# Kernel tuning notes

Hardware: AMD Instinct MI355X
Metric: run time of the kernel (lower is better)

Reference implementation:

```python
import jax, jax.numpy as jnp
import numpy as np

E = 1024   # embed_dim
H = 16     # num_heads
D = E // H # head_dim = 64
Q = 4      # num_queries
B = 4
S = 2048


def setup_inputs() -> dict:
    key = jax.random.key(0)
    ks = jax.random.split(key, 9)
    s = 0.02  # init scale for weights
    return {
        "x":  jax.random.normal(ks[0], (B, S, E), jnp.float32),
        "Wq": jax.random.normal(ks[1], (Q, E, E), jnp.float32) * s,  # stacked per-query Linear weights (torch layout: out,in)
        "bq": jax.random.normal(ks[2], (Q, E), jnp.float32) * s,
        "Wk": jax.random.normal(ks[3], (E, E), jnp.float32) * s,
        "bk": jax.random.normal(ks[4], (E,), jnp.float32) * s,
        "Wv": jax.random.normal(ks[5], (E, E), jnp.float32) * s,
        "bv": jax.random.normal(ks[6], (E,), jnp.float32) * s,
        "Wo": jax.random.normal(ks[7], (E, E), jnp.float32) * s,
        "bo": jax.random.normal(ks[8], (E,), jnp.float32) * s,
    }


def reference(x, Wq, bq, Wk, bk, Wv, bv, Wo, bo):
    B_, S_, E_ = x.shape
    scale = 1.0 / jnp.sqrt(jnp.asarray(D, x.dtype))
    # all query projections at once: (Q,B,S,E) -> (Q,B,S,H,D)
    q = (jnp.einsum('bse,qfe->qbsf', x, Wq) + bq[:, None, None, :]).reshape(Q, B_, S_, H, D)
    k = (x @ Wk.T + bk).reshape(B_, S_, H, D)
    v = (x @ Wv.T + bv).reshape(B_, S_, H, D)
    # NOTE: faithful to the torch code, which never moves the head axis before matmul:
    # scores[q,b,s,h,g] = sum_d q[q,b,s,h,d] * k[b,s,g,d]  -> softmax over heads g
    scores = jnp.einsum('qbshd,bsgd->qbshg', q, k) * scale      # (Q,B,S,H,H)
    probs = jax.nn.softmax(scores, axis=-1)
    out = jnp.einsum('qbshg,bsgd->qbshd', probs, v)             # (Q,B,S,H,D)
    # torch: .transpose(1,2).contiguous().view(B,S,E) == permute to (B,H,S,D) then reshape
    out = jnp.transpose(out, (0, 1, 3, 2, 4)).reshape(Q, B_, S_, E_)
    out = out.sum(axis=0)
    return out @ Wo.T + bo
```

## Files before the change

kernel.cpp:

```cpp
#include <hip/hip_runtime.h>


typedef __bf16 bf16x8 __attribute__((ext_vector_type(8)));
typedef float f32x4 __attribute__((ext_vector_type(4)));
typedef float f32x16 __attribute__((ext_vector_type(16)));

__device__ __forceinline__ unsigned short f2b(float f) {
  unsigned u = __float_as_uint(f);
  return (unsigned short)((u + 0x7fffu + ((u >> 16) & 1u)) >> 16);
}

__device__ __forceinline__ void async16(const void* g, void* l) {
  __builtin_amdgcn_global_load_lds(
      (const __attribute__((address_space(1))) void*)g,
      (__attribute__((address_space(3))) void*)l, 16, 0, 0);
}

__global__ __launch_bounds__(256) void cvt_all(
    const float* __restrict__ x, const float* __restrict__ Wq, const float* __restrict__ Wk,
    const float* __restrict__ Wv, const float* __restrict__ Wo, const float* __restrict__ bq,
    const float* __restrict__ bk, const float* __restrict__ bv,
    unsigned short* __restrict__ xb, unsigned short* __restrict__ wcat,
    unsigned short* __restrict__ wo_b, float* __restrict__ biascat) {
  if (blockIdx.x >= 15360) {
    int j = (blockIdx.x - 15360) * 256 + threadIdx.x;
    if (j < 6144) {
      float v = (j < 4096) ? bq[j] : (j < 5120 ? bk[j - 4096] : bv[j - 5120]);
      biascat[j] = v;
    }
    return;
  }
  int i = blockIdx.x * 256 + threadIdx.x;
  const float* s;
  unsigned short* d;
  int off;
  if (i < 2097152)      { s = x;  d = xb;             off = i; }
  else if (i < 3145728) { s = Wq; d = wcat;           off = i - 2097152; }
  else if (i < 3407872) { s = Wk; d = wcat + 4194304; off = i - 3145728; }
  else if (i < 3670016) { s = Wv; d = wcat + 5242880; off = i - 3407872; }
  else                  { s = Wo; d = wo_b;           off = i - 3670016; }
  float4 v = ((const float4*)s)[off];
  uint2 o;
  o.x = (unsigned)f2b(v.x) | ((unsigned)f2b(v.y) << 16);
  o.y = (unsigned)f2b(v.z) | ((unsigned)f2b(v.w) << 16);
  ((uint2*)d)[off] = o;
}

template <typename OutT>
__global__ __launch_bounds__(256) void gemm_bt(const unsigned short* __restrict__ A,
                                               const unsigned short* __restrict__ Bt,
                                               const float* __restrict__ bias,
                                               OutT* __restrict__ C, int M, int N, int K) {
  __shared__ __align__(16) unsigned short As[128 * 64];
  __shared__ __align__(16) unsigned short Bs[128 * 64];
  const int t = threadIdx.x;
  const int lane = t & 63, w = t >> 6;
  const int wm = (w >> 1) * 64, wn = (w & 1) * 64;
  const int l31 = lane & 31, lhi = lane >> 5;
  const int bm0 = blockIdx.y * 128, bn0 = blockIdx.x * 128;

  f32x16 acc[2][2];
#pragma unroll
  for (int i = 0; i < 2; ++i)
#pragma unroll
    for (int j = 0; j < 2; ++j)
#pragma unroll
      for (int e = 0; e < 16; ++e) acc[i][j][e] = 0.f;

  const int swz = l31 & 7;
  const int qoff = 2 * ((l31 >> 4) & 1);

  for (int k0 = 0; k0 < K; k0 += 64) {
    __syncthreads();
#pragma unroll
    for (int j = 0; j < 4; ++j) {
      int slot = j * 256 + t;
      int r = slot >> 3;
      int p = slot & 7;
      int c = (((p ^ (r & 7)) - 2 * ((r >> 4) & 1)) & 7) * 8;
      async16(A + (size_t)(bm0 + r) * K + k0 + c, As + slot * 8);
      async16(Bt + (size_t)(bn0 + r) * K + k0 + c, Bs + slot * 8);
    }
    __syncthreads();
#pragma unroll
    for (int kk = 0; kk < 64; kk += 16) {
      const int kg = kk >> 3;
      const int pg = ((((kg + lhi + qoff) & 7) ^ swz) << 3);
      bf16x8 af[2], bfr[2];
#pragma unroll
      for (int i = 0; i < 2; ++i)
        af[i] = *(const bf16x8*)(As + (wm + i * 32 + l31) * 64 + pg);
#pragma unroll
      for (int j = 0; j < 2; ++j)
        bfr[j] = *(const bf16x8*)(Bs + (wn + j * 32 + l31) * 64 + pg);
#pragma unroll
      for (int i = 0; i < 2; ++i)
#pragma unroll
        for (int j = 0; j < 2; ++j)
          acc[i][j] = __builtin_amdgcn_mfma_f32_32x32x16_bf16(af[i], bfr[j], acc[i][j], 0, 0, 0);
    }
  }

#pragma unroll
  for (int i = 0; i < 2; ++i) {
#pragma unroll
    for (int j = 0; j < 2; ++j) {
      int gc = bn0 + wn + j * 32 + l31;
      float bsv = bias[gc];
#pragma unroll
      for (int reg = 0; reg < 16; ++reg) {
        int gr = bm0 + wm + i * 32 + (reg & 3) + 8 * (reg >> 2) + 4 * lhi;
        float vv = acc[i][j][reg] + bsv;
        if constexpr (sizeof(OutT) == 2)
          C[(size_t)gr * N + gc] = (OutT)f2b(vv);
        else
          C[(size_t)gr * N + gc] = vv;
      }
    }
  }
}

__global__ __launch_bounds__(256) void attn_scatter(const unsigned short* __restrict__ qkv,
                                                    unsigned short* __restrict__ t) {
  __shared__ __align__(16) unsigned short vs[4][1024];
  __shared__ float ps[4][16 * 17];
  const int w = threadIdx.x >> 6, lane = threadIdx.x & 63;
  const int pos = blockIdx.x * 4 + w;
  const int b = pos >> 11, s = pos & 2047;
  const unsigned short* row = qkv + (size_t)pos * 6144;
  unsigned short* vw = vs[w];
  float* pw = ps[w];
  const int lr = lane & 15, lq = lane >> 4;

  {
    const uint4* sv = (const uint4*)(row + 5120);
    uint4* dv = (uint4*)vw;
    dv[lane * 2] = sv[lane * 2];
    dv[lane * 2 + 1] = sv[lane * 2 + 1];
  }
  bf16x8 kf0 = *(const bf16x8*)(row + 4096 + lr * 64 + lq * 8);
  bf16x8 kf1 = *(const bf16x8*)(row + 4096 + lr * 64 + 32 + lq * 8);

  bf16x8 vf[4];
#pragma unroll
  for (int dc = 0; dc < 4; ++dc) {
#pragma unroll
    for (int j = 0; j < 8; ++j) vf[dc][j] = (__bf16)0.0f;
    if (lq < 2) {
      const __bf16* vb = (const __bf16*)vw;
#pragma unroll
      for (int j = 0; j < 8; ++j)
        vf[dc][j] = vb[(lq * 8 + j) * 64 + dc * 16 + lr];
    }
  }

  f32x4 acc[4];
#pragma unroll
  for (int dc = 0; dc < 4; ++dc) acc[dc] = (f32x4){0.f, 0.f, 0.f, 0.f};

#pragma unroll
  for (int qi = 0; qi < 4; ++qi) {
    bf16x8 qf0 = *(const bf16x8*)(row + qi * 1024 + lr * 64 + lq * 8);
    bf16x8 qf1 = *(const bf16x8*)(row + qi * 1024 + lr * 64 + 32 + lq * 8);
    f32x4 sc = {0.f, 0.f, 0.f, 0.f};
    sc = __builtin_amdgcn_mfma_f32_16x16x32_bf16(qf0, kf0, sc, 0, 0, 0);
    sc = __builtin_amdgcn_mfma_f32_16x16x32_bf16(qf1, kf1, sc, 0, 0, 0);
#pragma unroll
    for (int r = 0; r < 4; ++r) {
      float e = __expf(sc[r] * 0.125f);
      float sum = e;
#pragma unroll
      for (int d = 1; d < 16; d <<= 1) sum += __shfl_xor(sum, d);
      pw[(lq * 4 + r) * 17 + lr] = e / sum;
    }
    bf16x8 pf;
#pragma unroll
    for (int j = 0; j < 8; ++j) pf[j] = (__bf16)0.0f;
    if (lq < 2) {
#pragma unroll
      for (int j = 0; j < 8; ++j) pf[j] = (__bf16)pw[lr * 17 + lq * 8 + j];
    }
#pragma unroll
    for (int dc = 0; dc < 4; ++dc)
      acc[dc] = __builtin_amdgcn_mfma_f32_16x16x32_bf16(vf[dc], pf, acc[dc], 0, 0, 0);
  }

  size_t base = ((size_t)(b * 2048 + 128 * lr + (s >> 4))) * 1024 + 64 * (s & 15) + lq * 4;
#pragma unroll
  for (int dc = 0; dc < 4; ++dc) {
    uint2 u;
    u.x = (unsigned)f2b(acc[dc][0]) | ((unsigned)f2b(acc[dc][1]) << 16);
    u.y = (unsigned)f2b(acc[dc][2]) | ((unsigned)f2b(acc[dc][3]) << 16);
    *(uint2*)(t + base + dc * 16) = u;
  }
}

extern "C" void kernel_launch(void* const* d_in, const int* in_sizes, int n_in,
                              void* d_out, int out_size, void* d_ws, size_t ws_size,
                              hipStream_t stream) {
  const float* x  = (const float*)d_in[0];
  const float* Wq = (const float*)d_in[1];
  const float* bq = (const float*)d_in[2];
  const float* Wk = (const float*)d_in[3];
  const float* bk = (const float*)d_in[4];
  const float* Wv = (const float*)d_in[5];
  const float* bv = (const float*)d_in[6];
  const float* Wo = (const float*)d_in[7];
  const float* bo = (const float*)d_in[8];
  float* out = (float*)d_out;

  char* ws = (char*)d_ws;
  unsigned short* xb      = (unsigned short*)(ws + 0);
  unsigned short* wcat    = (unsigned short*)(ws + 16777216);
  unsigned short* wo_b    = (unsigned short*)(ws + 29360128);
  float*          biascat = (float*)(ws + 31457280);
  unsigned short* qkv     = (unsigned short*)(ws + 31481856);
  unsigned short* t       = xb;

  cvt_all<<<15384, 256, 0, stream>>>(x, Wq, Wk, Wv, Wo, bq, bk, bv, xb, wcat, wo_b, biascat);

  gemm_bt<unsigned short><<<dim3(48, 64), 256, 0, stream>>>(xb, wcat, biascat, qkv, 8192, 6144, 1024);
  attn_scatter<<<2048, 256, 0, stream>>>(qkv, t);
  gemm_bt<float><<<dim3(8, 64), 256, 0, stream>>>(t, wo_b, bo, out, 8192, 1024, 1024);
}
```

Baseline: 277.9 us.

## Replace QKV projection GEMM with 256x256 tiled, 4-stage async-pipelined kernel

Adds a new GEMM kernel for the big QKV projection with 256x256 block tiles, 8 waves, and a 4-buffer LDS ring. Global-to-LDS async loads are issued two k-steps ahead and interleaved between halves of the MFMA work, using explicit vmcnt waits, barriers and setprio. The goal is more data reuse per tile and hiding memory latency behind MFMA compute. In exchange it uses more LDS and registers per block and needs hand-tuned synchronization, which limits occupancy and gives fewer blocks per CU.

After: 291.3 us. +4.8%, slower.

```diff
diff --git a/kernel.cpp b/kernel.cpp
--- a/kernel.cpp
+++ b/kernel.cpp
@@ -46,6 +46,123 @@
   ((uint2*)d)[off] = o;
 }
 
+__global__ __launch_bounds__(512, 2) void gemm256(
+    const unsigned short* __restrict__ A, const unsigned short* __restrict__ Bt,
+    const float* __restrict__ bias, unsigned short* __restrict__ C,
+    int M, int N, int K) {
+  __shared__ __align__(16) unsigned short As[4][8192];
+  __shared__ __align__(16) unsigned short Bs[4][8192];
+  const int t = threadIdx.x;
+  const int lane = t & 63, w = t >> 6;
+  const int l31 = lane & 31, lhi = lane >> 5;
+  const int wm = (w >> 2) * 128, wn = (w & 3) * 64;
+  const int bm0 = blockIdx.y * 256, bn0 = blockIdx.x * 256;
+
+  const int rA = t >> 2;
+  const int gA = ((t & 3) ^ (rA & 3)) * 8;
+  const unsigned short* aS = A + (size_t)(bm0 + rA) * K + gA;
+  const unsigned short* bS = Bt + (size_t)(bn0 + rA) * K + gA;
+  const size_t rowK128 = (size_t)128 * K;
+  const int d0 = t * 8, d1 = d0 + 4096;
+
+  const int swz = l31 & 3;
+  const int kc0 = (lhi ^ swz) * 8;
+  const int kc1 = ((2 + lhi) ^ swz) * 8;
+  int roA[4], roB[2];
+#pragma unroll
+  for (int mi = 0; mi < 4; ++mi) roA[mi] = (wm + mi * 32 + l31) * 32;
+#pragma unroll
+  for (int nj = 0; nj < 2; ++nj) roB[nj] = (wn + nj * 32 + l31) * 32;
+
+  f32x16 acc[4][2];
+#pragma unroll
+  for (int mi = 0; mi < 4; ++mi)
+#pragma unroll
+    for (int nj = 0; nj < 2; ++nj)
+#pragma unroll
+      for (int e = 0; e < 16; ++e) acc[mi][nj][e] = 0.f;
+
+#define STG_A(kt_) do { const int b_ = (kt_) & 3; const int ko_ = (kt_) * 32; \
+    async16(aS + ko_, &As[b_][d0]); async16(aS + rowK128 + ko_, &As[b_][d1]); } while (0)
+#define STG_B(kt_) do { const int b_ = (kt_) & 3; const int ko_ = (kt_) * 32; \
+    async16(bS + ko_, &Bs[b_][d0]); async16(bS + rowK128 + ko_, &Bs[b_][d1]); } while (0)
+
+  const int NT = K >> 5;
+  STG_A(0); STG_B(0); STG_A(1); STG_B(1);
+  asm volatile("s_waitcnt vmcnt(4)" ::: "memory");
+  asm volatile("s_barrier" ::: "memory");
+
+  for (int kt = 0; kt < NT; ++kt) {
+    const int bi = kt & 3;
+    const unsigned short* as_ = As[bi];
+    const unsigned short* bs_ = Bs[bi];
+
+    bf16x8 a0[2][2], bb[2][2];
+#pragma unroll
+    for (int mi = 0; mi < 2; ++mi) {
+      a0[mi][0] = *(const bf16x8*)(as_ + roA[mi] + kc0);
+      a0[mi][1] = *(const bf16x8*)(as_ + roA[mi] + kc1);
+    }
+#pragma unroll
+    for (int nj = 0; nj < 2; ++nj) {
+      bb[nj][0] = *(const bf16x8*)(bs_ + roB[nj] + kc0);
+      bb[nj][1] = *(const bf16x8*)(bs_ + roB[nj] + kc1);
+    }
+    if (kt + 2 < NT) { STG_A(kt + 2); }
+    asm volatile("s_barrier" ::: "memory");
+    __builtin_amdgcn_s_setprio(1);
+#pragma unroll
+    for (int mi = 0; mi < 2; ++mi)
+#pragma unroll
+      for (int nj = 0; nj < 2; ++nj) {
+        acc[mi][nj] = __builtin_amdgcn_mfma_f32_32x32x16_bf16(a0[mi][0], bb[nj][0], acc[mi][nj], 0, 0, 0);
+        acc[mi][nj] = __builtin_amdgcn_mfma_f32_32x32x16_bf16(a0[mi][1], bb[nj][1], acc[mi][nj], 0, 0, 0);
+      }
+    __builtin_amdgcn_s_setprio(0);
+    asm volatile("s_barrier" ::: "memory");
+
+    bf16x8 a1[2][2];
+#pragma unroll
+    for (int mi = 0; mi < 2; ++mi) {
+      a1[mi][0] = *(const bf16x8*)(as_ + roA[2 + mi] + kc0);
+      a1[mi][1] = *(const bf16x8*)(as_ + roA[2 + mi] + kc1);
+    }
+    if (kt + 2 < NT) { STG_B(kt + 2); }
+    asm volatile("s_barrier" ::: "memory");
+    __builtin_amdgcn_s_setprio(1);
+#pragma unroll
+    for (int mi = 0; mi < 2; ++mi)
+#pragma unroll
+      for (int nj = 0; nj < 2; ++nj) {
+        acc[2 + mi][nj] = __builtin_amdgcn_mfma_f32_32x32x16_bf16(a1[mi][0], bb[nj][0], acc[2 + mi][nj], 0, 0, 0);
+        acc[2 + mi][nj] = __builtin_amdgcn_mfma_f32_32x32x16_bf16(a1[mi][1], bb[nj][1], acc[2 + mi][nj], 0, 0, 0);
+      }
+    __builtin_amdgcn_s_setprio(0);
+    if (kt + 2 < NT) {
+      asm volatile("s_waitcnt vmcnt(4)" ::: "memory");
+    } else if (kt + 1 < NT) {
+      asm volatile("s_waitcnt vmcnt(0)" ::: "memory");
+    }
+    asm volatile("s_barrier" ::: "memory");
+  }
+#undef STG_A
+#undef STG_B
+
+#pragma unroll
+  for (int mi = 0; mi < 4; ++mi) {
+#pragma unroll
+    for (int nj = 0; nj < 2; ++nj) {
+      int gc = bn0 + wn + nj * 32 + l31;
+      float bsv = bias[gc];
+#pragma unroll
+      for (int reg = 0; reg < 16; ++reg) {
+        int gr = bm0 + wm + mi * 32 + (reg & 3) + 8 * (reg >> 2) + 4 * lhi;
+        C[(size_t)gr * N + gc] = f2b(acc[mi][nj][reg] + bsv);
+      }
+    }
+  }
+}
+
 template <typename OutT>
 __global__ __launch_bounds__(256) void gemm_bt(const unsigned short* __restrict__ A,
                                                const unsigned short* __restrict__ Bt,
@@ -219,7 +336,7 @@
 
   cvt_all<<<15384, 256, 0, stream>>>(x, Wq, Wk, Wv, Wo, bq, bk, bv, xb, wcat, wo_b, biascat);
 
-  gemm_bt<unsigned short><<<dim3(48, 64), 256, 0, stream>>>(xb, wcat, biascat, qkv, 8192, 6144, 1024);
+  gemm256<<<dim3(24, 32), 512, 0, stream>>>(xb, wcat, biascat, qkv, 8192, 6144, 1024);
   attn_scatter<<<2048, 256, 0, stream>>>(qkv, t);
   gemm_bt<float><<<dim3(8, 64), 256, 0, stream>>>(t, wo_b, bo, out, 8192, 1024, 1024);
 }
```

## Replace QKV projection GEMM with double-buffered 256x256 tile kernel

Applied to the files above, without the earlier changes.

Adds a new QKV projection GEMM with 256x256 output tiles and 512 threads. It double-buffers LDS across 128-wide K steps and interleaves async global-to-LDS loads with MFMA phases, using explicit barriers, waitcnt and setprio. The aim is to raise data reuse per tile and hide global load latency behind matrix math in the largest GEMM. In exchange it uses 128KB of LDS per block and many more accumulator registers, which can lower occupancy, and the hand-scheduled barriers are fragile.

New measurement: 290.5 us. 4.5% more time.

```diff
diff --git a/kernel.cpp b/kernel.cpp
--- a/kernel.cpp
+++ b/kernel.cpp
@@ -46,6 +46,213 @@
   ((uint2*)d)[off] = o;
 }
 
+__global__ __launch_bounds__(512, 2) void gemm256(
+    const unsigned short* __restrict__ A, const unsigned short* __restrict__ Bt,
+    const float* __restrict__ bias, unsigned short* __restrict__ C,
+    int M, int N, int K) {
+  __shared__ __align__(16) unsigned short As[2][16384];
+  __shared__ __align__(16) unsigned short Bs[2][16384];
+  const int t = threadIdx.x;
+  const int lane = t & 63, w = t >> 6;
+  const int l31 = lane & 31, lhi = lane >> 5;
+  const int wm = (w >> 2) * 128, wn = (w & 3) * 64;
+  const int bm0 = blockIdx.y * 256, bn0 = blockIdx.x * 256;
+  unsigned short* As0 = &As[0][0];
+  unsigned short* As1 = &As[1][0];
+  unsigned short* Bs0 = &Bs[0][0];
+  unsigned short* Bs1 = &Bs[1][0];
+
+  const int r0 = t >> 3;
+  const int p8 = (t & 7) * 8;
+  const int gsw = ((t & 7) ^ (r0 & 7)) * 8;
+  const int rb = ((r0 >> 5) << 6) + (r0 & 31);
+  const unsigned short* aG = A + (size_t)bm0 * K;
+  const unsigned short* bG = Bt + (size_t)bn0 * K;
+
+#define STG2(G_, L_, ra_, rb_, kt_) do {                                  \
+    const size_t ko_ = (size_t)(kt_) * 64 + gsw;                          \
+    async16(G_ + (size_t)(ra_) * K + ko_, L_ + (ra_) * 64 + p8);          \
+    async16(G_ + (size_t)(rb_) * K + ko_, L_ + (rb_) * 64 + p8);          \
+  } while (0)
+#define MFMA(a_, b_, c_) c_ = __builtin_amdgcn_mfma_f32_32x32x16_bf16(a_, b_, c_, 0, 0, 0)
+#define BAR() asm volatile("s_barrier" ::: "memory")
+#define WAIT_LDS() do { asm volatile("s_waitcnt lgkmcnt(0)" ::: "memory"); \
+    __builtin_amdgcn_sched_barrier(0); } while (0)
+
+  int prA[4], prB[2], pg[4];
+#pragma unroll
+  for (int mi = 0; mi < 4; ++mi) prA[mi] = (wm + mi * 32 + l31) * 64;
+#pragma unroll
+  for (int nj = 0; nj < 2; ++nj) prB[nj] = (wn + nj * 32 + l31) * 64;
+#pragma unroll
+  for (int ks = 0; ks < 4; ++ks) pg[ks] = ((2 * ks + lhi) ^ (l31 & 7)) * 8;
+
+  f32x16 acc[4][2];
+#pragma unroll
+  for (int mi = 0; mi < 4; ++mi)
+#pragma unroll
+    for (int nj = 0; nj < 2; ++nj)
+#pragma unroll
+      for (int e = 0; e < 16; ++e) acc[mi][nj][e] = 0.f;
+
+  const int NI = K >> 7;
+  STG2(aG, As0, r0, r0 + 128, 0);
+  STG2(aG, As0, r0 + 64, r0 + 192, 0);
+  STG2(bG, Bs0, rb, rb + 128, 0);
+  STG2(bG, Bs0, rb + 32, rb + 160, 0);
+  STG2(aG, As1, r0, r0 + 128, 1);
+  STG2(bG, Bs1, rb, rb + 128, 1);
+  STG2(bG, Bs1, rb + 32, rb + 160, 1);
+  asm volatile("s_waitcnt vmcnt(6)" ::: "memory");
+  BAR();
+
+  for (int i = 0; i < NI; ++i) {
+    const bool pf = (i + 1 < NI);
+    {
+      STG2(aG, As1, r0 + 64, r0 + 192, 2 * i + 1);
+      bf16x8 a01[2][4], b0[4];
+#pragma unroll
+      for (int ks = 0; ks < 4; ++ks) {
+        a01[0][ks] = *(const bf16x8*)(As0 + prA[0] + pg[ks]);
+        a01[1][ks] = *(const bf16x8*)(As0 + prA[1] + pg[ks]);
+        b0[ks]     = *(const bf16x8*)(Bs0 + prB[0] + pg[ks]);
+      }
+      BAR(); WAIT_LDS();
+      __builtin_amdgcn_s_setprio(1);
+#pragma unroll
+      for (int ks = 0; ks < 4; ++ks) {
+        MFMA(a01[0][ks], b0[ks], acc[0][0]);
+        MFMA(a01[1][ks], b0[ks], acc[1][0]);
+      }
+      __builtin_amdgcn_s_setprio(0);
+      BAR();
+
+      if (pf) STG2(aG, As0, r0, r0 + 128, 2 * i + 2);
+      bf16x8 b1[4];
+#pragma unroll
+      for (int ks = 0; ks < 4; ++ks) b1[ks] = *(const bf16x8*)(Bs0 + prB[1] + pg[ks]);
+      BAR(); WAIT_LDS();
+      __builtin_amdgcn_s_setprio(1);
+#pragma unroll
+      for (int ks = 0; ks < 4; ++ks) {
+        MFMA(a01[0][ks], b1[ks], acc[0][1]);
+        MFMA(a01[1][ks], b1[ks], acc[1][1]);
+      }
+      __builtin_amdgcn_s_setprio(0);
+      BAR();
+
+      if (pf) STG2(bG, Bs0, rb, rb + 128, 2 * i + 2);
+      bf16x8 a23[2][4];
+#pragma unroll
+      for (int ks = 0; ks < 4; ++ks) {
+        a23[0][ks] = *(const bf16x8*)(As0 + prA[2] + pg[ks]);
+        a23[1][ks] = *(const bf16x8*)(As0 + prA[3] + pg[ks]);
+      }
+      BAR(); WAIT_LDS();
+      __builtin_amdgcn_s_setprio(1);
+#pragma unroll
+      for (int ks = 0; ks < 4; ++ks) {
+        MFMA(a23[0][ks], b1[ks], acc[2][1]);
+        MFMA(a23[1][ks], b1[ks], acc[3][1]);
+      }
+      __builtin_amdgcn_s_setprio(0);
+      BAR();
+
+      if (pf) STG2(bG, Bs0, rb + 32, rb + 160, 2 * i + 2);
+      __builtin_amdgcn_s_setprio(1);
+#pragma unroll
+      for (int ks = 0; ks < 4; ++ks) {
+        MFMA(a23[0][ks], b0[ks], acc[2][0]);
+        MFMA(a23[1][ks], b0[ks], acc[3][0]);
+      }
+      __builtin_amdgcn_s_setprio(0);
+      if (pf) asm volatile("s_waitcnt vmcnt(6)" ::: "memory");
+      else    asm volatile("s_waitcnt vmcnt(0)" ::: "memory");
+      BAR();
+    }
+    {
+      if (pf) STG2(aG, As0, r0 + 64, r0 + 192, 2 * i + 2);
+      bf16x8 a01[2][4], b0[4];
+#pragma unroll
+      for (int ks = 0; ks < 4; ++ks) {
+        a01[0][ks] = *(const bf16x8*)(As1 + prA[0] + pg[ks]);
+        a01[1][ks] = *(const bf16x8*)(As1 + prA[1] + pg[ks]);
+        b0[ks]     = *(const bf16x8*)(Bs1 + prB[0] + pg[ks]);
+      }
+      BAR(); WAIT_LDS();
+      __builtin_amdgcn_s_setprio(1);
+#pragma unroll
+      for (int ks = 0; ks < 4; ++ks) {
+        MFMA(a01[0][ks], b0[ks], acc[0][0]);
+        MFMA(a01[1][ks], b0[ks], acc[1][0]);
+      }
+      __builtin_amdgcn_s_setprio(0);
+      BAR();
+
+      if (pf) STG2(aG, As1, r0, r0 + 128, 2 * i + 3);
+      bf16x8 b1[4];
+#pragma unroll
+      for (int ks = 0; ks < 4; ++ks) b1[ks] = *(const bf16x8*)(Bs1 + prB[1] + pg[ks]);
+      BAR(); WAIT_LDS();
+      __builtin_amdgcn_s_setprio(1);
+#pragma unroll
+      for (int ks = 0; ks < 4; ++ks) {
+        MFMA(a01[0][ks], b1[ks], acc[0][1]);
+        MFMA(a01[1][ks], b1[ks], acc[1][1]);
+      }
+      __builtin_amdgcn_s_setprio(0);
+      BAR();
+
+      if (pf) STG2(bG, Bs1, rb, rb + 128, 2 * i + 3);
+      bf16x8 a23[2][4];
+#pragma unroll
+      for (int ks = 0; ks < 4; ++ks) {
+        a23[0][ks] = *(const bf16x8*)(As1 + prA[2] + pg[ks]);
+        a23[1][ks] = *(const bf16x8*)(As1 + prA[3] + pg[ks]);
+      }
+      BAR(); WAIT_LDS();
+      __builtin_amdgcn_s_setprio(1);
+#pragma unroll
+      for (int ks = 0; ks < 4; ++ks) {
+        MFMA(a23[0][ks], b1[ks], acc[2][1]);
+        MFMA(a23[1][ks], b1[ks], acc[3][1]);
+      }
+      __builtin_amdgcn_s_setprio(0);
+      BAR();
+
+      if (pf) STG2(bG, Bs1, rb + 32, rb + 160, 2 * i + 3);
+      __builtin_amdgcn_s_setprio(1);
+#pragma unroll
+      for (int ks = 0; ks < 4; ++ks) {
+        MFMA(a23[0][ks], b0[ks], acc[2][0]);
+        MFMA(a23[1][ks], b0[ks], acc[3][0]);
+      }
+      __builtin_amdgcn_s_setprio(0);
+      if (pf) asm volatile("s_waitcnt vmcnt(6)" ::: "memory");
+      else    asm volatile("s_waitcnt vmcnt(0)" ::: "memory");
+      BAR();
+    }
+  }
+#undef STG2
+#undef MFMA
+#undef BAR
+#undef WAIT_LDS
+
+#pragma unroll
+  for (int mi = 0; mi < 4; ++mi) {
+#pragma unroll
+    for (int nj = 0; nj < 2; ++nj) {
+      int gc = bn0 + wn + nj * 32 + l31;
+      float bsv = bias[gc];
+#pragma unroll
+      for (int reg = 0; reg < 16; ++reg) {
+        int gr = bm0 + wm + mi * 32 + (reg & 3) + 8 * (reg >> 2) + 4 * lhi;
+        C[(size_t)gr * N + gc] = f2b(acc[mi][nj][reg] + bsv);
+      }
+    }
+  }
+}
+
 template <typename OutT>
 __global__ __launch_bounds__(256) void gemm_bt(const unsigned short* __restrict__ A,
                                                const unsigned short* __restrict__ Bt,
@@ -219,7 +426,7 @@
 
   cvt_all<<<15384, 256, 0, stream>>>(x, Wq, Wk, Wv, Wo, bq, bk, bv, xb, wcat, wo_b, biascat);
 
-  gemm_bt<unsigned short><<<dim3(48, 64), 256, 0, stream>>>(xb, wcat, biascat, qkv, 8192, 6144, 1024);
+  gemm256<<<dim3(24, 32), 512, 0, stream>>>(xb, wcat, biascat, qkv, 8192, 6144, 1024);
   attn_scatter<<<2048, 256, 0, stream>>>(qkv, t);
   gemm_bt<float><<<dim3(8, 64), 256, 0, stream>>>(t, wo_b, bo, out, 8192, 1024, 1024);
 }
```
